# Optimization experiments

Measured on AMD Instinct MI355X. Metric: run time of the kernel, lower is better.

The kernel has to match this reference:

```python
import jax, jax.numpy as jnp
import numpy as np


def _nearest_down(x, oh, ow):
    # torch F.interpolate(mode='nearest'): src_idx = floor(dst_idx * in/out)
    ih, iw = x.shape[-2], x.shape[-1]
    hi = jnp.floor(jnp.arange(oh) * (ih / oh)).astype(jnp.int32)
    wi = jnp.floor(jnp.arange(ow) * (iw / ow)).astype(jnp.int32)
    return x[..., hi, :][..., :, wi]


def setup_inputs() -> dict:
    key = jax.random.key(0)
    k1, k2, k3, k4 = jax.random.split(key, 4)
    B, Cf, Hf, Wf = 8, 256, 128, 128   # encoder feature map (stride 4)
    HL, WL = 512, 512                  # label / logit resolution
    C_OLD, NUM_CLASSES = 16, 21
    return {
        "outputs": jnp.zeros((1,), jnp.float32),        # overwritten in original forward
        "outputs_old": jax.random.normal(k1, (B, C_OLD, HL, WL), jnp.float32),
        "features": jax.random.normal(k2, (B, Cf, Hf, Wf), jnp.float32),
        "features_old": jnp.zeros((1,), jnp.float32),   # unused by this branch
        "labels": jax.random.randint(k3, (B, HL, WL), 0, NUM_CLASSES),
        "prototypes": jax.random.normal(k4, (NUM_CLASSES, Cf), jnp.float32),
        "classes_old": 16,
        "incremental_step": 1,
    }


def reference(outputs, outputs_old, features, features_old, labels, prototypes,
              classes_old, incremental_step):
    # Default branch: val=False, sequential=False, loss_de_prototypes_sumafter=False.
    if incremental_step == 0:
        return jnp.asarray(0.0, jnp.float32)
    B, C, H, W = features.shape
    # downsample labels to feature resolution (nearest)
    labels_down = _nearest_down(labels[:, None, :, :], H, W)      # [B,1,H,W] int
    bgr_mask = labels_down == 0
    # old-model pseudo-labels, masked to background of current labels
    pred_old = jnp.argmax(outputs_old, axis=1, keepdims=True)      # [B,1,HL,WL]
    pred_old_down = _nearest_down(pred_old, H, W)                  # [B,1,H,W]
    pseudo = jnp.where(bgr_mask, pred_old_down, 0)                 # [B,1,H,W]

    ids = pseudo.reshape(-1)                                       # [N]
    feats = jnp.transpose(features, (0, 2, 3, 1)).reshape(-1, C)   # [N,C]
    proto = jax.lax.stop_gradient(prototypes)                      # .detach()

    # per-pixel MSE (mean over channels) vs the prototype of its pseudo-class
    per_pix = jnp.mean(jnp.square(feats - proto[ids]), axis=-1)    # [N]

    sums = jax.ops.segment_sum(per_pix, ids, num_segments=classes_old)
    counts = jax.ops.segment_sum(jnp.ones_like(per_pix), ids, num_segments=classes_old)
    # mean over pixels of each present class; absent classes contribute 0
    per_class = jnp.where(counts > 0, sums / jnp.maximum(counts, 1.0), 0.0)
    # class 0 is excluded (cl_present drops background)
    return jnp.sum(per_class[1:])
```

## Files before the change

### kernel.cpp

```cpp
#include <hip/hip_runtime.h>

#define BB    8
#define CF    256
#define HF    128
#define WF    128
#define HLBL  512
#define WLBL  512
#define COLD  16
#define NCLS  21
#define PSTR  260


__global__ __launch_bounds__(256) void proto_loss_main(
    const float* __restrict__ outputs_old,
    const float* __restrict__ features,
    const int*   __restrict__ labels,
    const float* __restrict__ prototypes,
    float* __restrict__ gbins)
{
    __shared__ float sproto[COLD * PSTR];
    __shared__ float spartial[8][WF];
    __shared__ int   sids[WF];
    __shared__ float ssum[16];
    __shared__ float scnt[16];

    const int t   = threadIdx.x;
    const int blk = blockIdx.x;
    const int b   = blk >> 7;
    const int h   = blk & (HF - 1);

    #pragma unroll
    for (int i = t; i < COLD * (CF / 4); i += 256) {
        const int r  = i >> 6;
        const int c4 = (i & 63) << 2;
        *(float4*)&sproto[r * PSTR + c4] =
            *(const float4*)&prototypes[r * CF + c4];
    }
    if (t < 16) { ssum[t] = 0.0f; scnt[t] = 0.0f; }

    if (t < WF) {
        const int w = t;
        int id = 0;
        const int lab = labels[(b * HLBL + h * 4) * WLBL + w * 4];
        if (lab == 0) {
            const float* po = outputs_old
                + ((size_t)b * COLD * HLBL + (size_t)h * 4) * WLBL + w * 4;
            float best = po[0];
            #pragma unroll
            for (int c = 1; c < COLD; ++c) {
                float v = po[(size_t)c * HLBL * WLBL];
                if (v > best) { best = v; id = c; }
            }
        }
        sids[w] = id;
    }
    __syncthreads();

    const int w4    = (t & 31) * 4;
    const int c_off = t >> 5;
    const int id0 = sids[w4 + 0];
    const int id1 = sids[w4 + 1];
    const int id2 = sids[w4 + 2];
    const int id3 = sids[w4 + 3];

    float a0 = 0.f, a1 = 0.f, a2 = 0.f, a3 = 0.f;
    if ((id0 | id1 | id2 | id3) != 0) {
        const float* pr0 = &sproto[id0 * PSTR];
        const float* pr1 = &sproto[id1 * PSTR];
        const float* pr2 = &sproto[id2 * PSTR];
        const float* pr3 = &sproto[id3 * PSTR];
        const float* fbase = features + ((size_t)b * CF * HF + h) * WF + w4;

        #pragma unroll 8
        for (int k = 0; k < 32; ++k) {
            const int c = k * 8 + c_off;
            const float4 f = *(const float4*)(fbase + (size_t)c * (HF * WF));
            float d0 = f.x - pr0[c]; a0 += d0 * d0;
            float d1 = f.y - pr1[c]; a1 += d1 * d1;
            float d2 = f.z - pr2[c]; a2 += d2 * d2;
            float d3 = f.w - pr3[c]; a3 += d3 * d3;
        }
    }
    spartial[c_off][w4 + 0] = a0;
    spartial[c_off][w4 + 1] = a1;
    spartial[c_off][w4 + 2] = a2;
    spartial[c_off][w4 + 3] = a3;
    __syncthreads();

    if (t < WF) {
        const int id = sids[t];
        if (id != 0) {
            float pp = 0.f;
            #pragma unroll
            for (int co = 0; co < 8; ++co) pp += spartial[co][t];
            pp *= (1.0f / CF);
            atomicAdd(&ssum[id], pp);
            atomicAdd(&scnt[id], 1.0f);
        }
    }
    __syncthreads();

    if (t < 16) {
        if (scnt[t] > 0.f) {
            atomicAdd(&gbins[t],      ssum[t]);
            atomicAdd(&gbins[16 + t], scnt[t]);
        }
    }
}

__global__ void proto_loss_final(const float* __restrict__ gbins,
                                 const int* __restrict__ classes_old,
                                 const int* __restrict__ inc_step,
                                 float* __restrict__ out)
{
    if (threadIdx.x == 0 && blockIdx.x == 0) {
        float r = 0.0f;
        if (*inc_step != 0) {
            int K = *classes_old;
            if (K > 16) K = 16;
            for (int id = 1; id < K; ++id) {
                float cnt = gbins[16 + id];
                if (cnt > 0.f) r += gbins[id] / cnt;
            }
        }
        out[0] = r;
    }
}

extern "C" void kernel_launch(void* const* d_in, const int* in_sizes, int n_in,
                              void* d_out, int out_size, void* d_ws, size_t ws_size,
                              hipStream_t stream)
{
    const float* outputs_old = (const float*)d_in[1];
    const float* features    = (const float*)d_in[2];
    const int*   labels      = (const int*)d_in[4];
    const float* prototypes  = (const float*)d_in[5];
    const int*   classes_old = (const int*)d_in[6];
    const int*   inc_step    = (const int*)d_in[7];

    float* gbins = (float*)d_ws;

    hipMemsetAsync(gbins, 0, 32 * sizeof(float), stream);

    dim3 grid(BB * HF);
    dim3 block(256);
    proto_loss_main<<<grid, block, 0, stream>>>(outputs_old, features, labels,
                                                prototypes, gbins);
    proto_loss_final<<<1, 64, 0, stream>>>(gbins, classes_old, inc_step,
                                           (float*)d_out);
}
```

Before: 260.2 us.

## Compact active pixel quads and replace global atomics with per-block partials

Builds a per-row list of 4-pixel groups that have a nonzero pseudo-label and assigns eight channel-slice threads to each active group, so only those groups issue feature loads and arithmetic. Each block now writes its 32 per-class sums and counts to a workspace slot instead of issuing global atomics, and the final kernel reduces all slots in parallel. This removes the memset when workspace is large enough, at the cost of an extra shared atomic and barrier and a larger final reduction.

```diff
diff --git a/kernel.cpp b/kernel.cpp
--- a/kernel.cpp
+++ b/kernel.cpp
@@ -9,6 +9,7 @@
 #define COLD  16
 #define NCLS  21
 #define PSTR  260
+#define NPART (BB * HF)
 
 
 __global__ __launch_bounds__(256) void proto_loss_main(
@@ -16,11 +17,14 @@
     const float* __restrict__ features,
     const int*   __restrict__ labels,
     const float* __restrict__ prototypes,
-    float* __restrict__ gbins)
+    float* __restrict__ gpart,
+    const int nparts)
 {
     __shared__ float sproto[COLD * PSTR];
     __shared__ float spartial[8][WF];
     __shared__ int   sids[WF];
+    __shared__ int   sglist[WF / 4];
+    __shared__ int   sgcount;
     __shared__ float ssum[16];
     __shared__ float scnt[16];
 
@@ -37,6 +41,7 @@
             *(const float4*)&prototypes[r * CF + c4];
     }
     if (t < 16) { ssum[t] = 0.0f; scnt[t] = 0.0f; }
+    if (t == 0) sgcount = 0;
 
     if (t < WF) {
         const int w = t;
@@ -56,21 +61,32 @@
     }
     __syncthreads();
 
-    const int w4    = (t & 31) * 4;
-    const int c_off = t >> 5;
-    const int id0 = sids[w4 + 0];
-    const int id1 = sids[w4 + 1];
-    const int id2 = sids[w4 + 2];
-    const int id3 = sids[w4 + 3];
+    if (t < WF / 4) {
+        const int w4 = t * 4;
+        if ((sids[w4] | sids[w4 + 1] | sids[w4 + 2] | sids[w4 + 3]) != 0) {
+            const int pos = atomicAdd(&sgcount, 1);
+            sglist[pos] = t;
+        }
+    }
+    __syncthreads();
 
-    float a0 = 0.f, a1 = 0.f, a2 = 0.f, a3 = 0.f;
-    if ((id0 | id1 | id2 | id3) != 0) {
+    const int m     = sgcount;
+    const int s     = t >> 3;
+    const int c_off = t & 7;
+    if (s < m) {
+        const int g  = sglist[s];
+        const int w4 = g * 4;
+        const int id0 = sids[w4 + 0];
+        const int id1 = sids[w4 + 1];
+        const int id2 = sids[w4 + 2];
+        const int id3 = sids[w4 + 3];
         const float* pr0 = &sproto[id0 * PSTR];
         const float* pr1 = &sproto[id1 * PSTR];
         const float* pr2 = &sproto[id2 * PSTR];
         const float* pr3 = &sproto[id3 * PSTR];
         const float* fbase = features + ((size_t)b * CF * HF + h) * WF + w4;
 
+        float a0 = 0.f, a1 = 0.f, a2 = 0.f, a3 = 0.f;
         #pragma unroll 8
         for (int k = 0; k < 32; ++k) {
             const int c = k * 8 + c_off;
@@ -80,11 +96,11 @@
             float d2 = f.z - pr2[c]; a2 += d2 * d2;
             float d3 = f.w - pr3[c]; a3 += d3 * d3;
         }
+        spartial[c_off][w4 + 0] = a0;
+        spartial[c_off][w4 + 1] = a1;
+        spartial[c_off][w4 + 2] = a2;
+        spartial[c_off][w4 + 3] = a3;
     }
-    spartial[c_off][w4 + 0] = a0;
-    spartial[c_off][w4 + 1] = a1;
-    spartial[c_off][w4 + 2] = a2;
-    spartial[c_off][w4 + 3] = a3;
     __syncthreads();
 
     if (t < WF) {
@@ -100,27 +116,50 @@
     }
     __syncthreads();
 
-    if (t < 16) {
-        if (scnt[t] > 0.f) {
-            atomicAdd(&gbins[t],      ssum[t]);
-            atomicAdd(&gbins[16 + t], scnt[t]);
+    if (t < 32) {
+        const float v = (t < 16) ? ssum[t] : scnt[t - 16];
+        if (nparts > 1) {
+            gpart[(size_t)blk * 32 + t] = v;
+        } else {
+            if (v != 0.f) atomicAdd(&gpart[t], v);
         }
     }
 }
 
-__global__ void proto_loss_final(const float* __restrict__ gbins,
-                                 const int* __restrict__ classes_old,
-                                 const int* __restrict__ inc_step,
-                                 float* __restrict__ out)
+__global__ __launch_bounds__(256) void proto_loss_final(
+    const float* __restrict__ gpart, const int nparts,
+    const int* __restrict__ classes_old,
+    const int* __restrict__ inc_step,
+    float* __restrict__ out)
 {
-    if (threadIdx.x == 0 && blockIdx.x == 0) {
+    __shared__ float sacc[8][32];
+    const int t     = threadIdx.x;
+    const int bin   = t & 31;
+    const int slice = t >> 5;
+
+    float acc = 0.f;
+    #pragma unroll 8
+    for (int i = slice; i < nparts; i += 8)
+        acc += gpart[(size_t)i * 32 + bin];
+    sacc[slice][bin] = acc;
+    __syncthreads();
+
+    if (t < 32) {
+        float v = 0.f;
+        #pragma unroll
+        for (int s2 = 0; s2 < 8; ++s2) v += sacc[s2][t];
+        sacc[0][t] = v;
+    }
+    __syncthreads();
+
+    if (t == 0) {
         float r = 0.0f;
         if (*inc_step != 0) {
             int K = *classes_old;
             if (K > 16) K = 16;
             for (int id = 1; id < K; ++id) {
-                float cnt = gbins[16 + id];
-                if (cnt > 0.f) r += gbins[id] / cnt;
+                const float cnt = sacc[0][16 + id];
+                if (cnt > 0.f) r += sacc[0][id] / cnt;
             }
         }
         out[0] = r;
@@ -138,14 +177,19 @@
     const int*   classes_old = (const int*)d_in[6];
     const int*   inc_step    = (const int*)d_in[7];
 
-    float* gbins = (float*)d_ws;
+    float* gpart = (float*)d_ws;
+    const size_t needed = (size_t)NPART * 32 * sizeof(float);
 
-    hipMemsetAsync(gbins, 0, 32 * sizeof(float), stream);
+    int nparts;
+    if (ws_size >= needed) {
+        nparts = NPART;
+    } else {
+        nparts = 1;
+        hipMemsetAsync(gpart, 0, 32 * sizeof(float), stream);
+    }
 
-    dim3 grid(BB * HF);
-    dim3 block(256);
-    proto_loss_main<<<grid, block, 0, stream>>>(outputs_old, features, labels,
-                                                prototypes, gbins);
-    proto_loss_final<<<1, 64, 0, stream>>>(gbins, classes_old, inc_step,
-                                           (float*)d_out);
+    proto_loss_main<<<dim3(NPART), dim3(256), 0, stream>>>(
+        outputs_old, features, labels, prototypes, gpart, nparts);
+    proto_loss_final<<<dim3(1), dim3(256), 0, stream>>>(
+        gpart, nparts, classes_old, inc_step, (float*)d_out);
 }
```

New measurement: 265.8 us. 1.02x slower.
